# Kernel optimization log

Hardware: AMD Instinct MI355X
Metric: run time of the kernel (lower is better)

Reference implementation:

```python
import jax, jax.numpy as jnp
import numpy as np

IN_CH = 384
OUT_CH = 384
EPS = 1e-5  # torch LayerNorm default


def setup_inputs() -> dict:
    key = jax.random.key(0)
    k1, k2, k3 = jax.random.split(key, 3)
    x = jax.random.normal(k1, (32, IN_CH, 64, 64), dtype=jnp.float32)
    # LayerNorm params (torch defaults: gamma=1, beta=0; randomize slightly for a stronger test)
    ln_weight = jnp.ones((IN_CH,), jnp.float32) + 0.01 * jax.random.normal(k2, (IN_CH,), jnp.float32)
    ln_bias = jnp.zeros((IN_CH,), jnp.float32)
    # Linear params, kaiming-uniform-ish scale
    bound = 1.0 / np.sqrt(IN_CH)
    W = jax.random.uniform(k3, (OUT_CH, IN_CH), jnp.float32, -bound, bound)
    b = jnp.zeros((OUT_CH,), jnp.float32)
    return {"x": x, "ln_weight": ln_weight, "ln_bias": ln_bias, "W": W, "b": b}


def reference(x, ln_weight, ln_bias, W, b):
    # x: [B, C, H, W] -> normalize over channel dim, project C->OUT_CH, GELU, back to NCHW
    xh = jnp.transpose(x, (0, 2, 3, 1))  # [B, H, W, C]
    mu = jnp.mean(xh, axis=-1, keepdims=True)
    var = jnp.mean(jnp.square(xh - mu), axis=-1, keepdims=True)
    xn = (xh - mu) * jax.lax.rsqrt(var + EPS) * ln_weight + ln_bias
    y = jnp.einsum('bhwc,oc->bhwo', xn, W) + b
    y = jax.nn.gelu(y, approximate=False)  # torch nn.GELU default is exact erf form
    return jnp.transpose(y, (0, 3, 1, 2))  # [B, OUT_CH, H, W]
```

## Files before the change

### kernel.cpp

```cpp
#include <hip/hip_runtime.h>
#include <hip/hip_bf16.h>
#include <cmath>

typedef float f32x4 __attribute__((ext_vector_type(4)));
typedef float f32x16 __attribute__((ext_vector_type(16)));
typedef __bf16 bf16x2 __attribute__((ext_vector_type(2)));
typedef __bf16 bf16x4 __attribute__((ext_vector_type(4)));
typedef __bf16 bf16x8 __attribute__((ext_vector_type(8)));

#define C_IN 384
#define C_OUT 384
#define SPB 4096
#define NPIX 131072
#define BP 64
#define LDK 392
#define ROW2 34

__global__ __launch_bounds__(128) void ppl_prep_kernel(const float* __restrict__ W,
                                                       const float* __restrict__ gamma,
                                                       const float* __restrict__ beta,
                                                       const float* __restrict__ bias,
                                                       __bf16* __restrict__ Wp,
                                                       __bf16* __restrict__ Wt,
                                                       float* __restrict__ t1,
                                                       float* __restrict__ t2) {
  const int o = blockIdx.x;
  const int t = threadIdx.x;
  const float* row = W + o * C_IN;
  float s1 = 0.f, s2 = 0.f;
  for (int c = t; c < C_IN; c += 128) {
    const float w = row[c];
    const __bf16 wq = (__bf16)(w * gamma[c]);
    Wp[o * C_IN + c] = wq;
    Wt[(((size_t)(o >> 5) * 48 + (c >> 3)) << 8) + ((o & 31) << 3) + (c & 7)] = wq;
    s1 += (float)wq;
    s2 += beta[c] * w;
  }
#pragma unroll
  for (int off = 32; off > 0; off >>= 1) {
    s1 += __shfl_down(s1, off);
    s2 += __shfl_down(s2, off);
  }
  __shared__ float red[2][2];
  if ((t & 63) == 0) { red[t >> 6][0] = s1; red[t >> 6][1] = s2; }
  __syncthreads();
  if (t == 0) {
    t1[o] = red[0][0] + red[1][0];
    t2[o] = red[0][1] + red[1][1] + bias[o];
  }
}

__device__ __forceinline__ float gelu_fast(float v) {
  const float u = 0.7978845608028654f * v * __builtin_fmaf(0.044715f * v, v, 1.0f);
  const float e = __expf(-2.0f * u);
  return v * __builtin_amdgcn_rcpf(1.0f + e);
}

__global__ __launch_bounds__(512) void ppl_stats_cast_kernel(const float* __restrict__ x,
                                                             __bf16* __restrict__ xb,
                                                             float* __restrict__ mu,
                                                             float* __restrict__ rs) {
  __shared__ float sS[8][256];
  __shared__ float sQ[8][256];
  const int tid = threadIdx.x;
  const int w = tid >> 6;
  const int lane = tid & 63;
  const int p0 = blockIdx.x * 256;
  const int b = p0 >> 12;
  const int s0 = p0 & 4095;
  const int c0 = w * 48;
  const float* xp = x + (((size_t)(b * C_IN + c0)) << 12) + s0 + 4 * lane;
  __bf16* xbp = xb + (((size_t)(b * C_IN + c0)) << 12) + s0 + 4 * lane;

  f32x4 ssv = {0.f, 0.f, 0.f, 0.f};
  f32x4 qqv = {0.f, 0.f, 0.f, 0.f};
#pragma unroll
  for (int i = 0; i < 48; i += 12) {
    f32x4 L[12];
#pragma unroll
    for (int j = 0; j < 12; ++j)
      L[j] = *reinterpret_cast<const f32x4*>(xp + ((size_t)(i + j) << 12));
#pragma unroll
    for (int j = 0; j < 12; ++j) {
      const f32x4 v = L[j];
      ssv += v;
      qqv += v * v;
      bf16x4 pk;
      pk[0] = (__bf16)v[0];
      pk[1] = (__bf16)v[1];
      pk[2] = (__bf16)v[2];
      pk[3] = (__bf16)v[3];
      *reinterpret_cast<bf16x4*>(xbp + ((size_t)(i + j) << 12)) = pk;
    }
  }
  *reinterpret_cast<f32x4*>(&sS[w][4 * lane]) = ssv;
  *reinterpret_cast<f32x4*>(&sQ[w][4 * lane]) = qqv;
  __syncthreads();
  if (tid < 256) {
    float st = 0.f, qt = 0.f;
#pragma unroll
    for (int r = 0; r < 8; ++r) {
      st += sS[r][tid];
      qt += sQ[r][tid];
    }
    const float m = st * (1.0f / C_IN);
    mu[p0 + tid] = m;
    rs[p0 + tid] = rsqrtf(qt * (1.0f / C_IN) - m * m + 1e-5f);
  }
}

__global__ __launch_bounds__(256, 4) void ppl_gemm3_kernel(const __bf16* __restrict__ xb,
                                                           const __bf16* __restrict__ Wt,
                                                           const float* __restrict__ mug,
                                                           const float* __restrict__ rsg,
                                                           const float* __restrict__ t1g,
                                                           const float* __restrict__ t2g,
                                                           float* __restrict__ out) {
  __shared__ __bf16 Xs[2][BP * ROW2];
  __shared__ float mu_s[BP];
  __shared__ float rs_s[BP];

  const int tid = threadIdx.x;
  const int w = tid >> 6;
  const int lane = tid & 63;
  const int col = lane & 31;
  const int hi = lane >> 5;
  const int wm = w >> 1;
  const int wn = w & 1;
  const int bid = blockIdx.x;
  const int og = bid & 1;
  const int pt = bid >> 1;
  const int p0 = pt * BP;
  const int b = p0 >> 12;
  const int s0 = p0 & 4095;

  if (tid < BP) {
    mu_s[tid] = mug[p0 + tid];
    rs_s[tid] = rsg[p0 + tid];
  }

  const int v = tid & 15;
  const int c2 = tid >> 4;
  const __bf16* xsrc = xb + (((size_t)(b * C_IN) + 2 * c2) << 12) + s0 + 4 * v;
  __bf16* xdst = &Xs[0][0] + (4 * v) * ROW2 + 2 * c2;

  const int otb = og * 6 + wn * 3;
  const __bf16* wt0 = Wt + (((size_t)(otb + 0) * 48 + hi) << 8) + col * 8;
  const __bf16* wt1 = Wt + (((size_t)(otb + 1) * 48 + hi) << 8) + col * 8;
  const __bf16* wt2 = Wt + (((size_t)(otb + 2) * 48 + hi) << 8) + col * 8;

  const __bf16* abase = &Xs[0][0] + (wm * 32 + col) * ROW2 + hi * 8;

  f32x16 acc[3];
#pragma unroll
  for (int n = 0; n < 3; ++n)
#pragma unroll
    for (int r = 0; r < 16; ++r) acc[n][r] = 0.f;

  bf16x4 sA, sB;
#define SLOAD(K)                                                    \
  {                                                                 \
    const __bf16* sp_ = xsrc + ((size_t)(K) << 12);                 \
    sA = *reinterpret_cast<const bf16x4*>(sp_);                     \
    sB = *reinterpret_cast<const bf16x4*>(sp_ + SPB);               \
  }
#define SWRITE(bi)                                                  \
  {                                                                 \
    __bf16* d_ = xdst + (bi) * (BP * ROW2);                         \
    _Pragma("unroll") for (int r_ = 0; r_ < 4; ++r_) {              \
      bf16x2 pr_;                                                   \
      pr_[0] = sA[r_];                                              \
      pr_[1] = sB[r_];                                              \
      *reinterpret_cast<bf16x2*>(d_ + r_ * ROW2) = pr_;             \
    }                                                               \
  }

  SLOAD(0);
  SWRITE(0);
  __syncthreads();

#pragma unroll 2
  for (int it = 0; it < 12; ++it) {
    if (it < 11) SLOAD(32 * (it + 1));

    const __bf16* ap = abase + (it & 1) * (BP * ROW2);
    const bf16x8 a0 = *reinterpret_cast<const bf16x8*>(ap);
    const bf16x8 a1 = *reinterpret_cast<const bf16x8*>(ap + 16);

    const int kofs = it * 1024;
    const bf16x8 b00 = *reinterpret_cast<const bf16x8*>(wt0 + kofs);
    const bf16x8 b01 = *reinterpret_cast<const bf16x8*>(wt1 + kofs);
    const bf16x8 b02 = *reinterpret_cast<const bf16x8*>(wt2 + kofs);
    const bf16x8 b10 = *reinterpret_cast<const bf16x8*>(wt0 + kofs + 512);
    const bf16x8 b11 = *reinterpret_cast<const bf16x8*>(wt1 + kofs + 512);
    const bf16x8 b12 = *reinterpret_cast<const bf16x8*>(wt2 + kofs + 512);

    acc[0] = __builtin_amdgcn_mfma_f32_32x32x16_bf16(a0, b00, acc[0], 0, 0, 0);
    acc[1] = __builtin_amdgcn_mfma_f32_32x32x16_bf16(a0, b01, acc[1], 0, 0, 0);
    acc[2] = __builtin_amdgcn_mfma_f32_32x32x16_bf16(a0, b02, acc[2], 0, 0, 0);
    acc[0] = __builtin_amdgcn_mfma_f32_32x32x16_bf16(a1, b10, acc[0], 0, 0, 0);
    acc[1] = __builtin_amdgcn_mfma_f32_32x32x16_bf16(a1, b11, acc[1], 0, 0, 0);
    acc[2] = __builtin_amdgcn_mfma_f32_32x32x16_bf16(a1, b12, acc[2], 0, 0, 0);

    if (it < 11) SWRITE((it + 1) & 1);
    __syncthreads();
  }
#undef SLOAD
#undef SWRITE

#pragma unroll
  for (int n = 0; n < 3; ++n) {
    const int o = og * 192 + wn * 96 + n * 32 + col;
    const float t1v = t1g[o];
    const float t2v = t2g[o];
    float* op = out + (((size_t)(b * C_OUT + o)) << 12) + s0 + wm * 32;
#pragma unroll
    for (int qd = 0; qd < 4; ++qd) {
      const int pr = qd * 8 + hi * 4;
      const f32x4 mu4 = *reinterpret_cast<const f32x4*>(&mu_s[wm * 32 + pr]);
      const f32x4 rs4 = *reinterpret_cast<const f32x4*>(&rs_s[wm * 32 + pr]);
      f32x4 y;
#pragma unroll
      for (int r = 0; r < 4; ++r) {
        const float val = rs4[r] * (acc[n][qd * 4 + r] - mu4[r] * t1v) + t2v;
        y[r] = gelu_fast(val);
      }
      *reinterpret_cast<f32x4*>(op + pr) = y;
    }
  }
}

__global__ __launch_bounds__(256, 3) void ppl_fused_kernel(const float* __restrict__ x,
                                                           const __bf16* __restrict__ Wp,
                                                           const float* __restrict__ t1g,
                                                           const float* __restrict__ t2g,
                                                           float* __restrict__ out) {
  __shared__ __bf16 Xs[BP][LDK];
  __shared__ float sS[4][BP];
  __shared__ float sQ[4][BP];
  __shared__ float mu_s[BP];
  __shared__ float rs_s[BP];

  const int tid = threadIdx.x;
  const int w = tid >> 6;
  const int lane = tid & 63;
  const int q = tid & 15;
  const int j = tid >> 4;
  const int col = lane & 31;
  const int hi = lane >> 5;
  const int p0 = blockIdx.x * BP;
  const int b = p0 >> 12;
  const int s0 = p0 & 4095;
  const int ob = w * 96;

  const float* xq = x + (size_t)b * (C_IN * SPB) + s0 + 4 * q;

  f32x4 LA[12], LB[12];
#pragma unroll
  for (int i = 0; i < 3; ++i)
#pragma unroll
    for (int m = 0; m < 4; ++m)
      LA[i * 4 + m] = *reinterpret_cast<const f32x4*>(xq + (size_t)(64 * i + 4 * j + m) * SPB);
#pragma unroll
  for (int i = 0; i < 3; ++i)
#pragma unroll
    for (int m = 0; m < 4; ++m)
      LB[i * 4 + m] = *reinterpret_cast<const f32x4*>(xq + (size_t)(64 * (i + 3) + 4 * j + m) * SPB);

  float ss[4] = {0.f, 0.f, 0.f, 0.f};
  float qq[4] = {0.f, 0.f, 0.f, 0.f};

#define PROCESS(L, ibase)                                                   \
  {                                                                         \
    _Pragma("unroll") for (int i = 0; i < 3; ++i) {                         \
      _Pragma("unroll") for (int r = 0; r < 4; ++r) {                       \
        const float f0 = L[i * 4 + 0][r];                                   \
        const float f1 = L[i * 4 + 1][r];                                   \
        const float f2 = L[i * 4 + 2][r];                                   \
        const float f3 = L[i * 4 + 3][r];                                   \
        ss[r] += (f0 + f1) + (f2 + f3);                                     \
        qq[r] += (f0 * f0 + f1 * f1) + (f2 * f2 + f3 * f3);                 \
        bf16x4 pk;                                                          \
        pk[0] = (__bf16)f0; pk[1] = (__bf16)f1;                             \
        pk[2] = (__bf16)f2; pk[3] = (__bf16)f3;                             \
        *reinterpret_cast<bf16x4*>(&Xs[4 * q + r][64 * ((ibase) + i) + 4 * j]) = pk; \
      }                                                                     \
    }                                                                       \
  }
  PROCESS(LA, 0)
  PROCESS(LB, 3)
#undef PROCESS

#pragma unroll
  for (int r = 0; r < 4; ++r) {
    ss[r] += __shfl_xor(ss[r], 16);
    ss[r] += __shfl_xor(ss[r], 32);
    qq[r] += __shfl_xor(qq[r], 16);
    qq[r] += __shfl_xor(qq[r], 32);
  }
  if (lane < 16) {
#pragma unroll
    for (int r = 0; r < 4; ++r) {
      sS[w][4 * lane + r] = ss[r];
      sQ[w][4 * lane + r] = qq[r];
    }
  }
  __syncthreads();
  if (tid < BP) {
    const float st = sS[0][tid] + sS[1][tid] + sS[2][tid] + sS[3][tid];
    const float qt = sQ[0][tid] + sQ[1][tid] + sQ[2][tid] + sQ[3][tid];
    const float m = st * (1.0f / C_IN);
    mu_s[tid] = m;
    rs_s[tid] = rsqrtf(qt * (1.0f / C_IN) - m * m + 1e-5f);
  }
  __syncthreads();

  const __bf16* wp0 = Wp + (size_t)(ob + col) * C_IN + hi * 8;
  const __bf16* wp1 = wp0 + 32 * C_IN;
  const __bf16* wp2 = wp0 + 64 * C_IN;
  const __bf16* xs0 = &Xs[col][hi * 8];
  const __bf16* xs1 = &Xs[32 + col][hi * 8];

  f32x16 acc[2][3];
#pragma unroll
  for (int m = 0; m < 2; ++m)
#pragma unroll
    for (int n = 0; n < 3; ++n)
#pragma unroll
      for (int r = 0; r < 16; ++r) acc[m][n][r] = 0.f;

#define LOADB(dst, kk)                                     \
  {                                                        \
    dst[0] = *reinterpret_cast<const bf16x8*>(wp0 + (kk)); \
    dst[1] = *reinterpret_cast<const bf16x8*>(wp1 + (kk)); \
    dst[2] = *reinterpret_cast<const bf16x8*>(wp2 + (kk)); \
  }
#define STEP(bb, kk)                                                                    \
  {                                                                                     \
    const bf16x8 a0 = *reinterpret_cast<const bf16x8*>(xs0 + (kk));                     \
    const bf16x8 a1 = *reinterpret_cast<const bf16x8*>(xs1 + (kk));                     \
    acc[0][0] = __builtin_amdgcn_mfma_f32_32x32x16_bf16(a0, bb[0], acc[0][0], 0, 0, 0); \
    acc[0][1] = __builtin_amdgcn_mfma_f32_32x32x16_bf16(a0, bb[1], acc[0][1], 0, 0, 0); \
    acc[0][2] = __builtin_amdgcn_mfma_f32_32x32x16_bf16(a0, bb[2], acc[0][2], 0, 0, 0); \
    acc[1][0] = __builtin_amdgcn_mfma_f32_32x32x16_bf16(a1, bb[0], acc[1][0], 0, 0, 0); \
    acc[1][1] = __builtin_amdgcn_mfma_f32_32x32x16_bf16(a1, bb[1], acc[1][1], 0, 0, 0); \
    acc[1][2] = __builtin_amdgcn_mfma_f32_32x32x16_bf16(a1, bb[2], acc[1][2], 0, 0, 0); \
  }
  {
    bf16x8 bA[3], bB[3];
    LOADB(bA, 0);
#pragma unroll
    for (int it = 0; it < 12; ++it) {
      const int k = it * 32;
      LOADB(bB, k + 16);
      STEP(bA, k);
      if (it < 11) LOADB(bA, k + 32);
      STEP(bB, k + 16);
    }
  }
#undef LOADB
#undef STEP

  const float t1v[3] = {t1g[ob + col], t1g[ob + 32 + col], t1g[ob + 64 + col]};
  const float t2v[3] = {t2g[ob + col], t2g[ob + 32 + col], t2g[ob + 64 + col]};
  float* outp = out + (((size_t)(b * C_OUT + ob + col)) << 12) + s0;
#pragma unroll
  for (int nf = 0; nf < 3; ++nf) {
    float* op = outp + ((size_t)nf << 17);
#pragma unroll
    for (int m = 0; m < 2; ++m) {
#pragma unroll
      for (int qd = 0; qd < 4; ++qd) {
        const int pr = m * 32 + qd * 8 + hi * 4;
        const f32x4 mu4 = *reinterpret_cast<const f32x4*>(&mu_s[pr]);
        const f32x4 rs4 = *reinterpret_cast<const f32x4*>(&rs_s[pr]);
        f32x4 y;
#pragma unroll
        for (int r = 0; r < 4; ++r) {
          const float val = rs4[r] * (acc[m][nf][qd * 4 + r] - mu4[r] * t1v[nf]) + t2v[nf];
          y[r] = gelu_fast(val);
        }
        *reinterpret_cast<f32x4*>(op + pr) = y;
      }
    }
  }
}

extern "C" void kernel_launch(void* const* d_in, const int* in_sizes, int n_in,
                              void* d_out, int out_size, void* d_ws, size_t ws_size,
                              hipStream_t stream) {
  const float* x = (const float*)d_in[0];
  const float* gamma = (const float*)d_in[1];
  const float* beta = (const float*)d_in[2];
  const float* W = (const float*)d_in[3];
  const float* bias = (const float*)d_in[4];
  float* out = (float*)d_out;

  __bf16* Wp = (__bf16*)d_ws;
  __bf16* Wt = Wp + C_OUT * C_IN;
  float* t1 = (float*)(Wt + C_OUT * C_IN);
  float* t2 = t1 + C_OUT;
  float* mu = t2 + C_OUT;
  float* rs = mu + NPIX;
  __bf16* xb = (__bf16*)(rs + NPIX);

  const size_t need = 2 * (size_t)C_OUT * C_IN * 2 + 2 * C_OUT * 4 +
                      2 * (size_t)NPIX * 4 + (size_t)NPIX * C_IN * 2;

  ppl_prep_kernel<<<C_OUT, 128, 0, stream>>>(W, gamma, beta, bias, Wp, Wt, t1, t2);

  if (ws_size >= need) {
    ppl_stats_cast_kernel<<<NPIX / 256, 512, 0, stream>>>(x, xb, mu, rs);
    ppl_gemm3_kernel<<<(NPIX / BP) * 2, 256, 0, stream>>>(xb, Wt, mu, rs, t1, t2, out);
  } else {
    ppl_fused_kernel<<<NPIX / BP, 256, 0, stream>>>(x, Wp, t1, t2, out);
  }
}
```

Before: 175.8 us.

## Triple-buffer LDS tiles, prefetch weights a step ahead, nontemporal output stores

The GEMM main loop now uses three LDS buffers for the activation tiles, with global loads issued two iterations ahead. Weight fragments are prefetched one iteration ahead into alternating register sets, and the barrier is a raw s_barrier with an lgkmcnt wait and a sched_barrier. The aim is to hide global-load latency behind the MFMAs, and the output stores are marked nontemporal to avoid polluting cache. The cost is more registers and LDS per block, which could reduce occupancy at the 4-blocks-per-CU launch bound.

```diff
diff --git a/kernel.cpp b/kernel.cpp
--- a/kernel.cpp
+++ b/kernel.cpp
@@ -109,14 +109,14 @@
   }
 }
 
-__global__ __launch_bounds__(256, 4) void ppl_gemm3_kernel(const __bf16* __restrict__ xb,
+__global__ __launch_bounds__(256, 4) void ppl_gemm4_kernel(const __bf16* __restrict__ xb,
                                                            const __bf16* __restrict__ Wt,
                                                            const float* __restrict__ mug,
                                                            const float* __restrict__ rsg,
                                                            const float* __restrict__ t1g,
                                                            const float* __restrict__ t2g,
                                                            float* __restrict__ out) {
-  __shared__ __bf16 Xs[2][BP * ROW2];
+  __shared__ __bf16 Xs[3][BP * ROW2];
   __shared__ float mu_s[BP];
   __shared__ float rs_s[BP];
 
@@ -149,64 +149,89 @@
   const __bf16* wt1 = Wt + (((size_t)(otb + 1) * 48 + hi) << 8) + col * 8;
   const __bf16* wt2 = Wt + (((size_t)(otb + 2) * 48 + hi) << 8) + col * 8;
 
-  const __bf16* abase = &Xs[0][0] + (wm * 32 + col) * ROW2 + hi * 8;
-
   f32x16 acc[3];
 #pragma unroll
   for (int n = 0; n < 3; ++n)
 #pragma unroll
     for (int r = 0; r < 16; ++r) acc[n][r] = 0.f;
 
-  bf16x4 sA, sB;
-#define SLOAD(K)                                                    \
-  {                                                                 \
-    const __bf16* sp_ = xsrc + ((size_t)(K) << 12);                 \
-    sA = *reinterpret_cast<const bf16x4*>(sp_);                     \
-    sB = *reinterpret_cast<const bf16x4*>(sp_ + SPB);               \
-  }
-#define SWRITE(bi)                                                  \
-  {                                                                 \
-    __bf16* d_ = xdst + (bi) * (BP * ROW2);                         \
-    _Pragma("unroll") for (int r_ = 0; r_ < 4; ++r_) {              \
-      bf16x2 pr_;                                                   \
-      pr_[0] = sA[r_];                                              \
-      pr_[1] = sB[r_];                                              \
-      *reinterpret_cast<bf16x2*>(d_ + r_ * ROW2) = pr_;             \
-    }                                                               \
-  }
-
-  SLOAD(0);
-  SWRITE(0);
-  __syncthreads();
-
-#pragma unroll 2
+  bf16x4 sA0, sB0, sA1, sB1;
+  bf16x8 bP[6], bQ[6];
+
+#define SLOAD(sa, sb, K)                                   \
+  {                                                        \
+    const __bf16* sp_ = xsrc + ((size_t)(K) << 12);        \
+    sa = *reinterpret_cast<const bf16x4*>(sp_);            \
+    sb = *reinterpret_cast<const bf16x4*>(sp_ + SPB);      \
+  }
+#define SWRITE(bi, sa, sb)                                 \
+  {                                                        \
+    __bf16* d_ = xdst + (bi) * (BP * ROW2);                \
+    _Pragma("unroll") for (int r_ = 0; r_ < 4; ++r_) {     \
+      bf16x2 pr_;                                          \
+      pr_[0] = sa[r_];                                     \
+      pr_[1] = sb[r_];                                     \
+      *reinterpret_cast<bf16x2*>(d_ + r_ * ROW2) = pr_;    \
+    }                                                      \
+  }
+#define LOADB(dst, IT)                                                         \
+  {                                                                            \
+    const int ko_ = (IT) * 1024;                                               \
+    dst[0] = *reinterpret_cast<const bf16x8*>(wt0 + ko_);                      \
+    dst[1] = *reinterpret_cast<const bf16x8*>(wt1 + ko_);                      \
+    dst[2] = *reinterpret_cast<const bf16x8*>(wt2 + ko_);                      \
+    dst[3] = *reinterpret_cast<const bf16x8*>(wt0 + ko_ + 512);                \
+    dst[4] = *reinterpret_cast<const bf16x8*>(wt1 + ko_ + 512);                \
+    dst[5] = *reinterpret_cast<const bf16x8*>(wt2 + ko_ + 512);                \
+  }
+#define COMPUTE(bi, bb)                                                             \
+  {                                                                                 \
+    const __bf16* ap_ = &Xs[0][0] + (bi) * (BP * ROW2) + (wm * 32 + col) * ROW2 + hi * 8; \
+    const bf16x8 a0_ = *reinterpret_cast<const bf16x8*>(ap_);                       \
+    const bf16x8 a1_ = *reinterpret_cast<const bf16x8*>(ap_ + 16);                  \
+    acc[0] = __builtin_amdgcn_mfma_f32_32x32x16_bf16(a0_, bb[0], acc[0], 0, 0, 0);  \
+    acc[1] = __builtin_amdgcn_mfma_f32_32x32x16_bf16(a0_, bb[1], acc[1], 0, 0, 0);  \
+    acc[2] = __builtin_amdgcn_mfma_f32_32x32x16_bf16(a0_, bb[2], acc[2], 0, 0, 0);  \
+    acc[0] = __builtin_amdgcn_mfma_f32_32x32x16_bf16(a1_, bb[3], acc[0], 0, 0, 0);  \
+    acc[1] = __builtin_amdgcn_mfma_f32_32x32x16_bf16(a1_, bb[4], acc[1], 0, 0, 0);  \
+    acc[2] = __builtin_amdgcn_mfma_f32_32x32x16_bf16(a1_, bb[5], acc[2], 0, 0, 0);  \
+  }
+#define KBARRIER()                                         \
+  {                                                        \
+    asm volatile("s_waitcnt lgkmcnt(0)" ::: "memory");     \
+    __builtin_amdgcn_s_barrier();                          \
+    __builtin_amdgcn_sched_barrier(0);                     \
+  }
+
+  SLOAD(sA0, sB0, 0);
+  SLOAD(sA1, sB1, 32);
+  SWRITE(0, sA0, sB0);
+  LOADB(bP, 0);
+  KBARRIER();
+
+#pragma unroll
   for (int it = 0; it < 12; ++it) {
-    if (it < 11) SLOAD(32 * (it + 1));
-
-    const __bf16* ap = abase + (it & 1) * (BP * ROW2);
-    const bf16x8 a0 = *reinterpret_cast<const bf16x8*>(ap);
-    const bf16x8 a1 = *reinterpret_cast<const bf16x8*>(ap + 16);
-
-    const int kofs = it * 1024;
-    const bf16x8 b00 = *reinterpret_cast<const bf16x8*>(wt0 + kofs);
-    const bf16x8 b01 = *reinterpret_cast<const bf16x8*>(wt1 + kofs);
-    const bf16x8 b02 = *reinterpret_cast<const bf16x8*>(wt2 + kofs);
-    const bf16x8 b10 = *reinterpret_cast<const bf16x8*>(wt0 + kofs + 512);
-    const bf16x8 b11 = *reinterpret_cast<const bf16x8*>(wt1 + kofs + 512);
-    const bf16x8 b12 = *reinterpret_cast<const bf16x8*>(wt2 + kofs + 512);
-
-    acc[0] = __builtin_amdgcn_mfma_f32_32x32x16_bf16(a0, b00, acc[0], 0, 0, 0);
-    acc[1] = __builtin_amdgcn_mfma_f32_32x32x16_bf16(a0, b01, acc[1], 0, 0, 0);
-    acc[2] = __builtin_amdgcn_mfma_f32_32x32x16_bf16(a0, b02, acc[2], 0, 0, 0);
-    acc[0] = __builtin_amdgcn_mfma_f32_32x32x16_bf16(a1, b10, acc[0], 0, 0, 0);
-    acc[1] = __builtin_amdgcn_mfma_f32_32x32x16_bf16(a1, b11, acc[1], 0, 0, 0);
-    acc[2] = __builtin_amdgcn_mfma_f32_32x32x16_bf16(a1, b12, acc[2], 0, 0, 0);
-
-    if (it < 11) SWRITE((it + 1) & 1);
-    __syncthreads();
+    if (it < 11) {
+      if (it & 1) { SWRITE((it + 1) % 3, sA0, sB0); }
+      else        { SWRITE((it + 1) % 3, sA1, sB1); }
+    }
+    if (it < 10) {
+      if (it & 1) { SLOAD(sA1, sB1, 32 * (it + 2)); }
+      else        { SLOAD(sA0, sB0, 32 * (it + 2)); }
+    }
+    if (it < 11) {
+      if (it & 1) { LOADB(bP, it + 1); }
+      else        { LOADB(bQ, it + 1); }
+    }
+    if (it & 1) { COMPUTE(it % 3, bQ); }
+    else        { COMPUTE(it % 3, bP); }
+    KBARRIER();
   }
 #undef SLOAD
 #undef SWRITE
+#undef LOADB
+#undef COMPUTE
+#undef KBARRIER
 
 #pragma unroll
   for (int n = 0; n < 3; ++n) {
@@ -225,7 +250,7 @@
         const float val = rs4[r] * (acc[n][qd * 4 + r] - mu4[r] * t1v) + t2v;
         y[r] = gelu_fast(val);
       }
-      *reinterpret_cast<f32x4*>(op + pr) = y;
+      __builtin_nontemporal_store(y, reinterpret_cast<f32x4*>(op + pr));
     }
   }
 }
@@ -411,7 +436,7 @@
 
   if (ws_size >= need) {
     ppl_stats_cast_kernel<<<NPIX / 256, 512, 0, stream>>>(x, xb, mu, rs);
-    ppl_gemm3_kernel<<<(NPIX / BP) * 2, 256, 0, stream>>>(xb, Wt, mu, rs, t1, t2, out);
+    ppl_gemm4_kernel<<<(NPIX / BP) * 2, 256, 0, stream>>>(xb, Wt, mu, rs, t1, t2, out);
   } else {
     ppl_fused_kernel<<<NPIX / BP, 256, 0, stream>>>(x, Wp, t1, t2, out);
   }
```

Result: slower. 228.6 us (+30.1%).

## Emit MFMA-fragment-ordered bf16 activations and drop LDS staging from GEMM

Applied to the files above, without the earlier changes.

The stats kernel now transposes each 32-pixel group through shared memory and writes the bf16 activations in the exact per-lane MFMA A-fragment order. The GEMM kernel then loads A fragments straight from global memory into registers with a 3-deep A and 2-deep B software pipeline, removing the LDS double buffer and per-iteration barriers. The cost is an LDS transpose with strided 16-bit reads in the first kernel, more registers (occupancy hint lowered to 3) and mu/rs read from global in the epilogue.

```diff
diff --git a/kernel.cpp b/kernel.cpp
--- a/kernel.cpp
+++ b/kernel.cpp
@@ -14,7 +14,7 @@
 #define NPIX 131072
 #define BP 64
 #define LDK 392
-#define ROW2 34
+#define P1ROW 36
 
 __global__ __launch_bounds__(128) void ppl_prep_kernel(const float* __restrict__ W,
                                                        const float* __restrict__ gamma,
@@ -56,70 +56,93 @@
   return v * __builtin_amdgcn_rcpf(1.0f + e);
 }
 
-__global__ __launch_bounds__(512) void ppl_stats_cast_kernel(const float* __restrict__ x,
-                                                             __bf16* __restrict__ xb,
+__global__ __launch_bounds__(256) void ppl_stats_frag_kernel(const float* __restrict__ x,
+                                                             __bf16* __restrict__ xT,
                                                              float* __restrict__ mu,
                                                              float* __restrict__ rs) {
-  __shared__ float sS[8][256];
-  __shared__ float sQ[8][256];
+  __shared__ __bf16 Xc[C_IN * P1ROW];
+  __shared__ float sS[4][8][4];
+  __shared__ float sQ[4][8][4];
+
   const int tid = threadIdx.x;
-  const int w = tid >> 6;
-  const int lane = tid & 63;
-  const int p0 = blockIdx.x * 256;
+  const int q = tid & 7;
+  const int cg = tid >> 3;
+  const int g = blockIdx.x;
+  const int p0 = g * 32;
   const int b = p0 >> 12;
   const int s0 = p0 & 4095;
-  const int c0 = w * 48;
-  const float* xp = x + (((size_t)(b * C_IN + c0)) << 12) + s0 + 4 * lane;
-  __bf16* xbp = xb + (((size_t)(b * C_IN + c0)) << 12) + s0 + 4 * lane;
+
+  const float* xp = x + (((size_t)(b * C_IN + cg)) << 12) + s0 + 4 * q;
+
+  f32x4 L[12];
+#pragma unroll
+  for (int ch = 0; ch < 12; ++ch)
+    L[ch] = *reinterpret_cast<const f32x4*>(xp + (((size_t)ch * 32) << 12));
 
   f32x4 ssv = {0.f, 0.f, 0.f, 0.f};
   f32x4 qqv = {0.f, 0.f, 0.f, 0.f};
 #pragma unroll
-  for (int i = 0; i < 48; i += 12) {
-    f32x4 L[12];
-#pragma unroll
-    for (int j = 0; j < 12; ++j)
-      L[j] = *reinterpret_cast<const f32x4*>(xp + ((size_t)(i + j) << 12));
-#pragma unroll
-    for (int j = 0; j < 12; ++j) {
-      const f32x4 v = L[j];
-      ssv += v;
-      qqv += v * v;
-      bf16x4 pk;
-      pk[0] = (__bf16)v[0];
-      pk[1] = (__bf16)v[1];
-      pk[2] = (__bf16)v[2];
-      pk[3] = (__bf16)v[3];
-      *reinterpret_cast<bf16x4*>(xbp + ((size_t)(i + j) << 12)) = pk;
-    }
-  }
-  *reinterpret_cast<f32x4*>(&sS[w][4 * lane]) = ssv;
-  *reinterpret_cast<f32x4*>(&sQ[w][4 * lane]) = qqv;
+  for (int ch = 0; ch < 12; ++ch) {
+    const f32x4 v = L[ch];
+    ssv += v;
+    qqv += v * v;
+    bf16x4 pk;
+    pk[0] = (__bf16)v[0];
+    pk[1] = (__bf16)v[1];
+    pk[2] = (__bf16)v[2];
+    pk[3] = (__bf16)v[3];
+    *reinterpret_cast<bf16x4*>(&Xc[(ch * 32 + cg) * P1ROW + 4 * q]) = pk;
+  }
+
+#pragma unroll
+  for (int r = 0; r < 4; ++r) {
+    ssv[r] += __shfl_xor(ssv[r], 8);
+    ssv[r] += __shfl_xor(ssv[r], 16);
+    ssv[r] += __shfl_xor(ssv[r], 32);
+    qqv[r] += __shfl_xor(qqv[r], 8);
+    qqv[r] += __shfl_xor(qqv[r], 16);
+    qqv[r] += __shfl_xor(qqv[r], 32);
+  }
+  const int wv = tid >> 6;
+  const int lane = tid & 63;
+  if (lane < 8) {
+#pragma unroll
+    for (int r = 0; r < 4; ++r) {
+      sS[wv][lane][r] = ssv[r];
+      sQ[wv][lane][r] = qqv[r];
+    }
+  }
   __syncthreads();
-  if (tid < 256) {
-    float st = 0.f, qt = 0.f;
-#pragma unroll
-    for (int r = 0; r < 8; ++r) {
-      st += sS[r][tid];
-      qt += sQ[r][tid];
-    }
+  if (tid < 32) {
+    const int qq_ = tid >> 2, rr_ = tid & 3;
+    const float st = sS[0][qq_][rr_] + sS[1][qq_][rr_] + sS[2][qq_][rr_] + sS[3][qq_][rr_];
+    const float qt = sQ[0][qq_][rr_] + sQ[1][qq_][rr_] + sQ[2][qq_][rr_] + sQ[3][qq_][rr_];
     const float m = st * (1.0f / C_IN);
     mu[p0 + tid] = m;
     rs[p0 + tid] = rsqrtf(qt * (1.0f / C_IN) - m * m + 1e-5f);
   }
-}
-
-__global__ __launch_bounds__(256, 4) void ppl_gemm3_kernel(const __bf16* __restrict__ xb,
+
+  const int px = lane & 31;
+  const int oct = lane >> 5;
+  __bf16* xto = xT + (size_t)g * 12288 + lane * 8;
+#pragma unroll
+  for (int i = 0; i < 6; ++i) {
+    const int f = wv * 6 + i;
+    const int cb = (f >> 1) * 32 + (f & 1) * 16 + oct * 8;
+    bf16x8 frag;
+#pragma unroll
+    for (int j = 0; j < 8; ++j) frag[j] = Xc[(cb + j) * P1ROW + px];
+    *reinterpret_cast<bf16x8*>(xto + (size_t)f * 512) = frag;
+  }
+}
+
+__global__ __launch_bounds__(256, 3) void ppl_gemm5_kernel(const __bf16* __restrict__ xT,
                                                            const __bf16* __restrict__ Wt,
                                                            const float* __restrict__ mug,
                                                            const float* __restrict__ rsg,
                                                            const float* __restrict__ t1g,
                                                            const float* __restrict__ t2g,
                                                            float* __restrict__ out) {
-  __shared__ __bf16 Xs[2][BP * ROW2];
-  __shared__ float mu_s[BP];
-  __shared__ float rs_s[BP];
-
   const int tid = threadIdx.x;
   const int w = tid >> 6;
   const int lane = tid & 63;
@@ -133,80 +156,67 @@
   const int p0 = pt * BP;
   const int b = p0 >> 12;
   const int s0 = p0 & 4095;
-
-  if (tid < BP) {
-    mu_s[tid] = mug[p0 + tid];
-    rs_s[tid] = rsg[p0 + tid];
-  }
-
-  const int v = tid & 15;
-  const int c2 = tid >> 4;
-  const __bf16* xsrc = xb + (((size_t)(b * C_IN) + 2 * c2) << 12) + s0 + 4 * v;
-  __bf16* xdst = &Xs[0][0] + (4 * v) * ROW2 + 2 * c2;
-
+  const int g = pt * 2 + wm;
+
+  const __bf16* aptr = xT + (size_t)g * 12288 + lane * 8;
   const int otb = og * 6 + wn * 3;
   const __bf16* wt0 = Wt + (((size_t)(otb + 0) * 48 + hi) << 8) + col * 8;
   const __bf16* wt1 = Wt + (((size_t)(otb + 1) * 48 + hi) << 8) + col * 8;
   const __bf16* wt2 = Wt + (((size_t)(otb + 2) * 48 + hi) << 8) + col * 8;
 
-  const __bf16* abase = &Xs[0][0] + (wm * 32 + col) * ROW2 + hi * 8;
-
   f32x16 acc[3];
 #pragma unroll
   for (int n = 0; n < 3; ++n)
 #pragma unroll
     for (int r = 0; r < 16; ++r) acc[n][r] = 0.f;
 
-  bf16x4 sA, sB;
-#define SLOAD(K)                                                    \
-  {                                                                 \
-    const __bf16* sp_ = xsrc + ((size_t)(K) << 12);                 \
-    sA = *reinterpret_cast<const bf16x4*>(sp_);                     \
-    sB = *reinterpret_cast<const bf16x4*>(sp_ + SPB);               \
-  }
-#define SWRITE(bi)                                                  \
-  {                                                                 \
-    __bf16* d_ = xdst + (bi) * (BP * ROW2);                         \
-    _Pragma("unroll") for (int r_ = 0; r_ < 4; ++r_) {              \
-      bf16x2 pr_;                                                   \
-      pr_[0] = sA[r_];                                              \
-      pr_[1] = sB[r_];                                              \
-      *reinterpret_cast<bf16x2*>(d_ + r_ * ROW2) = pr_;             \
-    }                                                               \
-  }
-
-  SLOAD(0);
-  SWRITE(0);
-  __syncthreads();
-
-#pragma unroll 2
+  bf16x8 aF0[3], aF1[3];
+  bf16x8 bS0[6], bS1[6];
+
+#define ALOAD(d, kt)                                                        \
+  {                                                                         \
+    aF0[d] = *reinterpret_cast<const bf16x8*>(aptr + (kt) * 1024);          \
+    aF1[d] = *reinterpret_cast<const bf16x8*>(aptr + (kt) * 1024 + 512);    \
+  }
+#define BLOAD(arr, kt)                                                      \
+  {                                                                         \
+    const int ko_ = (kt) * 1024;                                            \
+    arr[0] = *reinterpret_cast<const bf16x8*>(wt0 + ko_);                   \
+    arr[1] = *reinterpret_cast<const bf16x8*>(wt1 + ko_);                   \
+    arr[2] = *reinterpret_cast<const bf16x8*>(wt2 + ko_);                   \
+    arr[3] = *reinterpret_cast<const bf16x8*>(wt0 + ko_ + 512);             \
+    arr[4] = *reinterpret_cast<const bf16x8*>(wt1 + ko_ + 512);             \
+    arr[5] = *reinterpret_cast<const bf16x8*>(wt2 + ko_ + 512);             \
+  }
+#define CSTEP(d, arr)                                                               \
+  {                                                                                 \
+    acc[0] = __builtin_amdgcn_mfma_f32_32x32x16_bf16(aF0[d], arr[0], acc[0], 0, 0, 0); \
+    acc[1] = __builtin_amdgcn_mfma_f32_32x32x16_bf16(aF0[d], arr[1], acc[1], 0, 0, 0); \
+    acc[2] = __builtin_amdgcn_mfma_f32_32x32x16_bf16(aF0[d], arr[2], acc[2], 0, 0, 0); \
+    acc[0] = __builtin_amdgcn_mfma_f32_32x32x16_bf16(aF1[d], arr[3], acc[0], 0, 0, 0); \
+    acc[1] = __builtin_amdgcn_mfma_f32_32x32x16_bf16(aF1[d], arr[4], acc[1], 0, 0, 0); \
+    acc[2] = __builtin_amdgcn_mfma_f32_32x32x16_bf16(aF1[d], arr[5], acc[2], 0, 0, 0); \
+  }
+
+  ALOAD(0, 0);
+  ALOAD(1, 1);
+  ALOAD(2, 2);
+  BLOAD(bS0, 0);
+  BLOAD(bS1, 1);
+
+#pragma unroll
   for (int it = 0; it < 12; ++it) {
-    if (it < 11) SLOAD(32 * (it + 1));
-
-    const __bf16* ap = abase + (it & 1) * (BP * ROW2);
-    const bf16x8 a0 = *reinterpret_cast<const bf16x8*>(ap);
-    const bf16x8 a1 = *reinterpret_cast<const bf16x8*>(ap + 16);
-
-    const int kofs = it * 1024;
-    const bf16x8 b00 = *reinterpret_cast<const bf16x8*>(wt0 + kofs);
-    const bf16x8 b01 = *reinterpret_cast<const bf16x8*>(wt1 + kofs);
-    const bf16x8 b02 = *reinterpret_cast<const bf16x8*>(wt2 + kofs);
-    const bf16x8 b10 = *reinterpret_cast<const bf16x8*>(wt0 + kofs + 512);
-    const bf16x8 b11 = *reinterpret_cast<const bf16x8*>(wt1 + kofs + 512);
-    const bf16x8 b12 = *reinterpret_cast<const bf16x8*>(wt2 + kofs + 512);
-
-    acc[0] = __builtin_amdgcn_mfma_f32_32x32x16_bf16(a0, b00, acc[0], 0, 0, 0);
-    acc[1] = __builtin_amdgcn_mfma_f32_32x32x16_bf16(a0, b01, acc[1], 0, 0, 0);
-    acc[2] = __builtin_amdgcn_mfma_f32_32x32x16_bf16(a0, b02, acc[2], 0, 0, 0);
-    acc[0] = __builtin_amdgcn_mfma_f32_32x32x16_bf16(a1, b10, acc[0], 0, 0, 0);
-    acc[1] = __builtin_amdgcn_mfma_f32_32x32x16_bf16(a1, b11, acc[1], 0, 0, 0);
-    acc[2] = __builtin_amdgcn_mfma_f32_32x32x16_bf16(a1, b12, acc[2], 0, 0, 0);
-
-    if (it < 11) SWRITE((it + 1) & 1);
-    __syncthreads();
-  }
-#undef SLOAD
-#undef SWRITE
+    if (it & 1) { CSTEP(it % 3, bS1); }
+    else        { CSTEP(it % 3, bS0); }
+    if (it + 3 < 12) ALOAD(it % 3, it + 3);
+    if (it + 2 < 12) {
+      if (it & 1) { BLOAD(bS1, it + 2); }
+      else        { BLOAD(bS0, it + 2); }
+    }
+  }
+#undef ALOAD
+#undef BLOAD
+#undef CSTEP
 
 #pragma unroll
   for (int n = 0; n < 3; ++n) {
@@ -217,8 +227,8 @@
 #pragma unroll
     for (int qd = 0; qd < 4; ++qd) {
       const int pr = qd * 8 + hi * 4;
-      const f32x4 mu4 = *reinterpret_cast<const f32x4*>(&mu_s[wm * 32 + pr]);
-      const f32x4 rs4 = *reinterpret_cast<const f32x4*>(&rs_s[wm * 32 + pr]);
+      const f32x4 mu4 = *reinterpret_cast<const f32x4*>(mug + p0 + wm * 32 + pr);
+      const f32x4 rs4 = *reinterpret_cast<const f32x4*>(rsg + p0 + wm * 32 + pr);
       f32x4 y;
 #pragma unroll
       for (int r = 0; r < 4; ++r) {
@@ -402,7 +412,7 @@
   float* t2 = t1 + C_OUT;
   float* mu = t2 + C_OUT;
   float* rs = mu + NPIX;
-  __bf16* xb = (__bf16*)(rs + NPIX);
+  __bf16* xT = (__bf16*)(rs + NPIX);
 
   const size_t need = 2 * (size_t)C_OUT * C_IN * 2 + 2 * C_OUT * 4 +
                       2 * (size_t)NPIX * 4 + (size_t)NPIX * C_IN * 2;
@@ -410,8 +420,8 @@
   ppl_prep_kernel<<<C_OUT, 128, 0, stream>>>(W, gamma, beta, bias, Wp, Wt, t1, t2);
 
   if (ws_size >= need) {
-    ppl_stats_cast_kernel<<<NPIX / 256, 512, 0, stream>>>(x, xb, mu, rs);
-    ppl_gemm3_kernel<<<(NPIX / BP) * 2, 256, 0, stream>>>(xb, Wt, mu, rs, t1, t2, out);
+    ppl_stats_frag_kernel<<<NPIX / 32, 256, 0, stream>>>(x, xT, mu, rs);
+    ppl_gemm5_kernel<<<(NPIX / BP) * 2, 256, 0, stream>>>(xT, Wt, mu, rs, t1, t2, out);
   } else {
     ppl_fused_kernel<<<NPIX / BP, 256, 0, stream>>>(x, Wp, t1, t2, out);
   }
```

After: 194.4 us. +10.6%, slower.
